# Kernel tuning notes

Measured on AMD Instinct MI355X. Metric: run time of the kernel, lower is better.

The kernel has to match this reference:

```python
import jax, jax.numpy as jnp
import numpy as np
import math

H = 2048      # hidden_size
NH = 32       # num heads
HD = H // NH  # head_dim = 64
THETA = 10000.0
B, S = 2, 2048


def _rope_tables(seq_len):
    inv_freq = 1.0 / (THETA ** (jnp.arange(0, HD, 2, dtype=jnp.float32) / HD))
    t = jnp.arange(seq_len, dtype=jnp.float32)
    freqs = t[:, None] * inv_freq[None, :]          # [S, HD/2]
    emb = jnp.concatenate([freqs, freqs], axis=-1)  # [S, HD]
    return jnp.cos(emb)[None, None], jnp.sin(emb)[None, None]  # [1,1,S,HD]


def _rotate_half(x):
    x1, x2 = jnp.split(x, 2, axis=-1)
    return jnp.concatenate([-x2, x1], axis=-1)


def setup_inputs() -> dict:
    key = jax.random.key(0)
    ks = jax.random.split(key, 5)
    hidden_states = jax.random.normal(ks[0], (B, S, H), dtype=jnp.float32)
    wscale = 1.0 / math.sqrt(H)
    wq = jax.random.normal(ks[1], (H, H), dtype=jnp.float32) * wscale
    wk = jax.random.normal(ks[2], (H, H), dtype=jnp.float32) * wscale
    wv = jax.random.normal(ks[3], (H, H), dtype=jnp.float32) * wscale
    wo = jax.random.normal(ks[4], (H, H), dtype=jnp.float32) * wscale
    # additive causal mask: 0 on/below diagonal, -1e9 above
    causal = jnp.tril(jnp.ones((S, S), dtype=bool))
    attention_mask = jnp.where(causal, 0.0, -1e9).astype(jnp.float32)[None, None]
    return {"hidden_states": hidden_states, "attention_mask": attention_mask,
            "wq": wq, "wk": wk, "wv": wv, "wo": wo}


def reference(hidden_states, attention_mask, wq, wk, wv, wo):
    b, s, _ = hidden_states.shape
    # projections (Linear, no bias); weights stored [in, out]
    q = (hidden_states @ wq).reshape(b, s, NH, HD).transpose(0, 2, 1, 3)  # [B,NH,S,HD]
    k = (hidden_states @ wk).reshape(b, s, NH, HD).transpose(0, 2, 1, 3)
    v = (hidden_states @ wv).reshape(b, s, NH, HD).transpose(0, 2, 1, 3)
    # RoPE
    cos, sin = _rope_tables(s)
    q = q * cos + _rotate_half(q) * sin
    k = k * cos + _rotate_half(k) * sin
    # attention
    attn = jnp.einsum('bhqd,bhkd->bhqk', q, k) / math.sqrt(HD)
    attn = attn + attention_mask
    w = jax.nn.softmax(attn, axis=-1)
    out = jnp.einsum('bhqk,bhkd->bhqd', w, v)           # [B,NH,S,HD]
    out = out.transpose(0, 2, 1, 3).reshape(b, s, H)    # [B,S,H]
    return out @ wo
```

## Files before the change

kernel.cpp:

```cpp
#include <hip/hip_runtime.h>
#include <hip/hip_bf16.h>

#define H 2048
#define NH 32
#define HD 64
#define BB 2
#define SS 2048
#define MM (BB*SS)

typedef __attribute__((ext_vector_type(8))) short bf16x8;
typedef __attribute__((ext_vector_type(4))) float f32x4;
typedef __attribute__((ext_vector_type(16))) float f32x16;
typedef unsigned short u16;
typedef unsigned int u32;
typedef __attribute__((ext_vector_type(4))) u32 u32x4;

static __device__ __forceinline__ u16 f2bf(float f){
  union { float f; u32 i; } v; v.f = f;
  u32 x = v.i;
  return (u16)((x + 0x7FFFu + ((x >> 16) & 1u)) >> 16);
}
static __device__ __forceinline__ float bf2f(u16 u){
  union { u32 i; float f; } v; v.i = ((u32)u) << 16; return v.f;
}
static __device__ __forceinline__ u32 pk2(float a, float b){
  u32 r;
  asm("v_cvt_pk_bf16_f32 %0, %1, %2" : "=v"(r) : "v"(a), "v"(b));
  return r;
}

static __device__ __forceinline__ void gload16(const u16* g, u16* l){
  __builtin_amdgcn_global_load_lds((const __attribute__((address_space(1))) void*)g,
                                   (__attribute__((address_space(3))) void*)l, 16, 0, 0);
}

__global__ void k_cvt(const float* __restrict__ src, u16* __restrict__ dst){
  const int i = (blockIdx.x * 256 + threadIdx.x) * 4;
  float4 v = *(const float4*)(src + i);
  ushort4 o;
  o.x = f2bf(v.x); o.y = f2bf(v.y); o.z = f2bf(v.z); o.w = f2bf(v.w);
  *(ushort4*)(dst + i) = o;
}

__global__ void k_wtrans(const float* __restrict__ w0, const float* __restrict__ w1,
                         const float* __restrict__ w2, const float* __restrict__ w3,
                         u16* __restrict__ d0, u16* __restrict__ d1,
                         u16* __restrict__ d2, u16* __restrict__ d3){
  __shared__ float tile[32][33];
  const int z = blockIdx.z;
  const float* w = z==0 ? w0 : z==1 ? w1 : z==2 ? w2 : w3;
  u16* d        = z==0 ? d0 : z==1 ? d1 : z==2 ? d2 : d3;
  const int n0 = blockIdx.x * 32, k0 = blockIdx.y * 32;
  const int tx = threadIdx.x, ty = threadIdx.y;
  #pragma unroll
  for (int j = 0; j < 4; j++)
    tile[ty + 8*j][tx] = w[(size_t)(k0 + ty + 8*j) * H + n0 + tx];
  __syncthreads();
  #pragma unroll
  for (int j = 0; j < 4; j++)
    d[(size_t)(n0 + ty + 8*j) * H + k0 + tx] = f2bf(tile[tx][ty + 8*j]);
}

__global__ __launch_bounds__(512, 2) void k_gemm8(
    const u16* __restrict__ A, const u16* __restrict__ Bt,
    u16* __restrict__ CQ, u16* __restrict__ CK, u16* __restrict__ CV,
    int M, int K){
  __shared__ __align__(16) u16 As[2][128][64];
  __shared__ __align__(16) u16 Bs[2][384][64];
  const int flat = blockIdx.x;
  const int id = (flat & 7) * 64 + (flat >> 3);
  const int gy = id >> 5, gx = id & 31;
  const int m0 = gx * 128, n0 = gy * 384;
  const int t = threadIdx.x, w = t >> 6, l = t & 63;
  const int wm = w >> 2, wn = w & 3;
  const int lrow = l & 15, lk = (l >> 4) * 8;
  const int sw = (lrow & 7) * 8;
  const int sr = t >> 3, sc = (t & 7) * 8;
  const int ssc = sc ^ ((sr & 7) * 8);
  const int NK = K >> 6;

  auto stageA = [&](int kt, int u){
    const size_t kb = (size_t)kt * 64 + ssc;
    #pragma unroll
    for (int c = 0; c < 2; c++)
      gload16(A + (size_t)(m0 + c*64 + sr) * K + kb, &As[u][c*64 + sr][sc]);
  };
  auto stageB = [&](int kt, int u){
    const size_t kb = (size_t)kt * 64 + ssc;
    #pragma unroll
    for (int c = 0; c < 6; c++)
      gload16(Bt + (size_t)(n0 + c*64 + sr) * K + kb, &Bs[u][c*64 + sr][sc]);
  };

  f32x4 acc[4][6] = {};

  stageA(0, 0); stageB(0, 0);
  stageA(1, 1); stageB(1, 1);
  asm volatile("s_waitcnt vmcnt(8)" ::: "memory");
  __builtin_amdgcn_s_barrier();

  #pragma unroll 1
  for (int kt = 0; kt < NK; ++kt){
    const int u = kt & 1;
    const bool more = (kt + 2 < NK);
    bf16x8 b0[6], b1[6], a0, a1;

    #pragma unroll
    for (int n = 0; n < 6; n++)
      b0[n] = *(const bf16x8*)&Bs[u][wn*96 + n*16 + lrow][lk ^ sw];
    a0 = *(const bf16x8*)&As[u][wm*64 +  0 + lrow][lk ^ sw];
    a1 = *(const bf16x8*)&As[u][wm*64 + 16 + lrow][lk ^ sw];
    __builtin_amdgcn_s_setprio(1);
    #pragma unroll
    for (int n = 0; n < 6; n++){
      acc[0][n] = __builtin_amdgcn_mfma_f32_16x16x32_bf16(a0, b0[n], acc[0][n], 0, 0, 0);
      acc[1][n] = __builtin_amdgcn_mfma_f32_16x16x32_bf16(a1, b0[n], acc[1][n], 0, 0, 0);
    }
    __builtin_amdgcn_s_setprio(0);
    __builtin_amdgcn_s_barrier();

    #pragma unroll
    for (int n = 0; n < 6; n++)
      b1[n] = *(const bf16x8*)&Bs[u][wn*96 + n*16 + lrow][(32 + lk) ^ sw];
    a0 = *(const bf16x8*)&As[u][wm*64 +  0 + lrow][(32 + lk) ^ sw];
    a1 = *(const bf16x8*)&As[u][wm*64 + 16 + lrow][(32 + lk) ^ sw];
    __builtin_amdgcn_s_setprio(1);
    #pragma unroll
    for (int n = 0; n < 6; n++){
      acc[0][n] = __builtin_amdgcn_mfma_f32_16x16x32_bf16(a0, b1[n], acc[0][n], 0, 0, 0);
      acc[1][n] = __builtin_amdgcn_mfma_f32_16x16x32_bf16(a1, b1[n], acc[1][n], 0, 0, 0);
    }
    __builtin_amdgcn_s_setprio(0);
    __builtin_amdgcn_s_barrier();

    if (more) stageB(kt + 2, u);
    a0 = *(const bf16x8*)&As[u][wm*64 + 32 + lrow][lk ^ sw];
    a1 = *(const bf16x8*)&As[u][wm*64 + 48 + lrow][lk ^ sw];
    __builtin_amdgcn_s_setprio(1);
    #pragma unroll
    for (int n = 0; n < 6; n++){
      acc[2][n] = __builtin_amdgcn_mfma_f32_16x16x32_bf16(a0, b0[n], acc[2][n], 0, 0, 0);
      acc[3][n] = __builtin_amdgcn_mfma_f32_16x16x32_bf16(a1, b0[n], acc[3][n], 0, 0, 0);
    }
    __builtin_amdgcn_s_setprio(0);
    __builtin_amdgcn_s_barrier();

    a0 = *(const bf16x8*)&As[u][wm*64 + 32 + lrow][(32 + lk) ^ sw];
    a1 = *(const bf16x8*)&As[u][wm*64 + 48 + lrow][(32 + lk) ^ sw];
    __builtin_amdgcn_s_setprio(1);
    #pragma unroll
    for (int n = 0; n < 6; n++){
      acc[2][n] = __builtin_amdgcn_mfma_f32_16x16x32_bf16(a0, b1[n], acc[2][n], 0, 0, 0);
      acc[3][n] = __builtin_amdgcn_mfma_f32_16x16x32_bf16(a1, b1[n], acc[3][n], 0, 0, 0);
    }
    __builtin_amdgcn_s_setprio(0);
    __builtin_amdgcn_s_barrier();

    if (more){
      stageA(kt + 2, u);
      asm volatile("s_waitcnt vmcnt(8)" ::: "memory");
      __builtin_amdgcn_s_barrier();
    } else if (kt + 1 < NK){
      asm volatile("s_waitcnt vmcnt(0)" ::: "memory");
      __builtin_amdgcn_s_barrier();
    }
  }

  #pragma unroll
  for (int m = 0; m < 4; m++)
    #pragma unroll
    for (int n = 0; n < 6; n++){
      const int ncol = n0 + wn*96 + n*16 + lrow;
      const int z = ncol >> 11;
      u16* C = (z == 0 ? CQ : z == 1 ? CK : CV) + (ncol & 2047);
      #pragma unroll
      for (int r = 0; r < 4; r++){
        const int row = m0 + wm*64 + m*16 + (l >> 4)*4 + r;
        C[(size_t)row * H] = f2bf(acc[m][n][r]);
      }
    }
}

__global__ __launch_bounds__(512, 2) void k_gemmo(
    const u16* __restrict__ A, const u16* __restrict__ Bt,
    float* __restrict__ C, int M, int N, int K){
  __shared__ __align__(16) u16 As[2][128][64];
  __shared__ __align__(16) u16 Bs[2][256][64];
  const int flat = blockIdx.x;
  const int id = (flat & 7) * 32 + (flat >> 3);
  const int gy = id >> 5, gx = id & 31;
  const int m0 = gx * 128, n0 = gy * 256;
  const int t = threadIdx.x, w = t >> 6, l = t & 63;
  const int wm = w >> 2, wn = w & 3;
  const int lrow = l & 15, lk = (l >> 4) * 8;
  const int sw = (lrow & 7) * 8;
  const int sr = t >> 3, sc = (t & 7) * 8;
  const int ssc = sc ^ ((sr & 7) * 8);
  const int NK = K >> 6;

  auto stageA = [&](int kt, int u){
    const size_t kb = (size_t)kt * 64 + ssc;
    #pragma unroll
    for (int c = 0; c < 2; c++)
      gload16(A + (size_t)(m0 + c*64 + sr) * K + kb, &As[u][c*64 + sr][sc]);
  };
  auto stageB = [&](int kt, int u){
    const size_t kb = (size_t)kt * 64 + ssc;
    #pragma unroll
    for (int c = 0; c < 4; c++)
      gload16(Bt + (size_t)(n0 + c*64 + sr) * K + kb, &Bs[u][c*64 + sr][sc]);
  };

  f32x4 acc[4][4] = {};

  stageA(0, 0); stageB(0, 0);
  stageA(1, 1); stageB(1, 1);
  asm volatile("s_waitcnt vmcnt(6)" ::: "memory");
  __builtin_amdgcn_s_barrier();

  #pragma unroll 1
  for (int kt = 0; kt < NK; ++kt){
    const int u = kt & 1;
    const bool more = (kt + 2 < NK);
    bf16x8 b0[4], b1[4], a0, a1;

    #pragma unroll
    for (int n = 0; n < 4; n++)
      b0[n] = *(const bf16x8*)&Bs[u][wn*64 + n*16 + lrow][lk ^ sw];
    a0 = *(const bf16x8*)&As[u][wm*64 +  0 + lrow][lk ^ sw];
    a1 = *(const bf16x8*)&As[u][wm*64 + 16 + lrow][lk ^ sw];
    __builtin_amdgcn_s_setprio(1);
    #pragma unroll
    for (int n = 0; n < 4; n++){
      acc[0][n] = __builtin_amdgcn_mfma_f32_16x16x32_bf16(a0, b0[n], acc[0][n], 0, 0, 0);
      acc[1][n] = __builtin_amdgcn_mfma_f32_16x16x32_bf16(a1, b0[n], acc[1][n], 0, 0, 0);
    }
    __builtin_amdgcn_s_setprio(0);
    __builtin_amdgcn_s_barrier();

    #pragma unroll
    for (int n = 0; n < 4; n++)
      b1[n] = *(const bf16x8*)&Bs[u][wn*64 + n*16 + lrow][(32 + lk) ^ sw];
    a0 = *(const bf16x8*)&As[u][wm*64 +  0 + lrow][(32 + lk) ^ sw];
    a1 = *(const bf16x8*)&As[u][wm*64 + 16 + lrow][(32 + lk) ^ sw];
    __builtin_amdgcn_s_setprio(1);
    #pragma unroll
    for (int n = 0; n < 4; n++){
      acc[0][n] = __builtin_amdgcn_mfma_f32_16x16x32_bf16(a0, b1[n], acc[0][n], 0, 0, 0);
      acc[1][n] = __builtin_amdgcn_mfma_f32_16x16x32_bf16(a1, b1[n], acc[1][n], 0, 0, 0);
    }
    __builtin_amdgcn_s_setprio(0);
    __builtin_amdgcn_s_barrier();

    if (more) stageB(kt + 2, u);
    a0 = *(const bf16x8*)&As[u][wm*64 + 32 + lrow][lk ^ sw];
    a1 = *(const bf16x8*)&As[u][wm*64 + 48 + lrow][lk ^ sw];
    __builtin_amdgcn_s_setprio(1);
    #pragma unroll
    for (int n = 0; n < 4; n++){
      acc[2][n] = __builtin_amdgcn_mfma_f32_16x16x32_bf16(a0, b0[n], acc[2][n], 0, 0, 0);
      acc[3][n] = __builtin_amdgcn_mfma_f32_16x16x32_bf16(a1, b0[n], acc[3][n], 0, 0, 0);
    }
    __builtin_amdgcn_s_setprio(0);
    __builtin_amdgcn_s_barrier();

    a0 = *(const bf16x8*)&As[u][wm*64 + 32 + lrow][(32 + lk) ^ sw];
    a1 = *(const bf16x8*)&As[u][wm*64 + 48 + lrow][(32 + lk) ^ sw];
    __builtin_amdgcn_s_setprio(1);
    #pragma unroll
    for (int n = 0; n < 4; n++){
      acc[2][n] = __builtin_amdgcn_mfma_f32_16x16x32_bf16(a0, b1[n], acc[2][n], 0, 0, 0);
      acc[3][n] = __builtin_amdgcn_mfma_f32_16x16x32_bf16(a1, b1[n], acc[3][n], 0, 0, 0);
    }
    __builtin_amdgcn_s_setprio(0);
    __builtin_amdgcn_s_barrier();

    if (more){
      stageA(kt + 2, u);
      asm volatile("s_waitcnt vmcnt(6)" ::: "memory");
      __builtin_amdgcn_s_barrier();
    } else if (kt + 1 < NK){
      asm volatile("s_waitcnt vmcnt(0)" ::: "memory");
      __builtin_amdgcn_s_barrier();
    }
  }

  #pragma unroll
  for (int m = 0; m < 4; m++)
    #pragma unroll
    for (int n = 0; n < 4; n++){
      const int col = n0 + wn*64 + n*16 + lrow;
      #pragma unroll
      for (int r = 0; r < 4; r++){
        const int row = m0 + wm*64 + m*16 + (l >> 4)*4 + r;
        C[(size_t)row * N + col] = acc[m][n][r];
      }
    }
}

__global__ void k_rope(u16* __restrict__ Kp){
  const int idx = blockIdx.x * 256 + threadIdx.x;
  const int quad = idx & 3;
  const int h = (idx >> 2) & 31;
  const int row = idx >> 7;
  const int s = row & (SS - 1);
  const int i0 = quad * 8;
  u16* k = Kp + (size_t)row * H + h * HD;
  uint4 k1v = *(const uint4*)(k + i0);
  uint4 k2v = *(const uint4*)(k + i0 + 32);
  u16* k1 = (u16*)&k1v; u16* k2 = (u16*)&k2v;
  const float sf = (float)s;
  #pragma unroll
  for (int e = 0; e < 8; e++){
    const int i = i0 + e;
    const float inv = exp2f(-0.4152410118609203f * (float)i);
    float rev = sf * inv * 0.15915494309189535f;
    rev -= floorf(rev);
    const float sn = __builtin_amdgcn_sinf(rev);
    const float cs = __builtin_amdgcn_cosf(rev);
    const float ka = bf2f(k1[e]), kb = bf2f(k2[e]);
    k1[e] = f2bf(ka*cs - kb*sn);
    k2[e] = f2bf(kb*cs + ka*sn);
  }
  *(uint4*)(k + i0)      = k1v;
  *(uint4*)(k + i0 + 32) = k2v;
}

__global__ __launch_bounds__(256, 2) void k_attn(
    const u16* __restrict__ Q, const u16* __restrict__ K,
    const u16* __restrict__ V, u16* __restrict__ O){
  __shared__ __align__(16) u16 Ks[3][64][64];
  __shared__ __align__(16) u16 Vs[2][64][72];
  const int t = threadIdx.x, w = t >> 6, l = t & 63;
  const int x = blockIdx.x, bh = blockIdx.y;
  const int b = bh >> 5, h = bh & 31;
  const u16* kp = K + (size_t)(b*SS) * H + h * HD;
  const u16* vp = V + (size_t)(b*SS) * H + h * HD;
  const int sr = t >> 3, sc = (t & 7) * 8;
  const int ssc = sc ^ ((sr & 7) * 8);
  const int hi = l >> 5, lq = l & 31;
  const float QSC = 0.18033688011112042f;

  auto stageK = [&](int tile, int buf){
    const int jb = tile * 64;
    gload16(kp + (size_t)(jb + sr) * H + ssc,      &Ks[buf][sr][sc]);
    gload16(kp + (size_t)(jb + 32 + sr) * H + ssc, &Ks[buf][32 + sr][sc]);
  };
  auto loadV = [&](int tile, uint4* vv){
    const int jb = tile * 64;
    vv[0] = *(const uint4*)(vp + (size_t)(jb + sr) * H + sc);
    vv[1] = *(const uint4*)(vp + (size_t)(jb + 32 + sr) * H + sc);
  };
  auto publishV = [&](const uint4* vv, int buf){
    #pragma unroll
    for (int c = 0; c < 2; c++){
      const int j = c*32 + sr;
      const u16* pv = (const u16*)&vv[c];
      #pragma unroll
      for (int e = 0; e < 8; e++){
        const int d = sc + e;
        Vs[buf][d][j ^ ((d >> 3) * 8)] = pv[e];
      }
    }
  };

  #pragma unroll 1
  for (int pp = 0; pp < 2; pp++){
    const int qt = pp ? x : (15 - x);
    const int NT = 2*qt + 2;
    const int qw0 = qt*128 + w*32;
    const int qrow = qw0 + lq;

    const u16* qptr = Q + (size_t)(b*SS + qrow) * H + h * HD + hi*8;
    bf16x8 qr0 = *(const bf16x8*)(qptr + 0);
    bf16x8 qr1 = *(const bf16x8*)(qptr + 16);
    bf16x8 qr2 = *(const bf16x8*)(qptr + 32);
    bf16x8 qr3 = *(const bf16x8*)(qptr + 48);
    bf16x8 qf[4];
    {
      const float sf = (float)qrow;
      #pragma unroll
      for (int e = 0; e < 8; e++){
        #pragma unroll
        for (int pr = 0; pr < 2; pr++){
          const int d = pr*16 + hi*8 + e;
          const float inv = exp2f(-0.4152410118609203f * (float)d);
          float rev = sf * inv * 0.15915494309189535f;
          rev -= floorf(rev);
          const float sn = __builtin_amdgcn_sinf(rev);
          const float cs = __builtin_amdgcn_cosf(rev);
          const float qa = bf2f((u16)(pr ? qr1[e] : qr0[e]));
          const float qb = bf2f((u16)(pr ? qr3[e] : qr2[e]));
          const u16 oa = f2bf((qa*cs - qb*sn) * QSC);
          const u16 ob = f2bf((qb*cs + qa*sn) * QSC);
          if (pr){ qf[1][e] = (short)oa; qf[3][e] = (short)ob; }
          else   { qf[0][e] = (short)oa; qf[2][e] = (short)ob; }
        }
      }
    }

    float mrun = -1e30f, lrun = 0.f;
    f32x16 oacc[2] = {};
    uint4 vvE[2], vvO[2];

    stageK(0, 0); loadV(0, vvE);
    stageK(1, 1); loadV(1, vvO);
    asm volatile("s_waitcnt vmcnt(4)" ::: "memory");
    publishV(vvE, 0);
    asm volatile("s_waitcnt lgkmcnt(0)" ::: "memory");
    __builtin_amdgcn_s_barrier();

    auto body = [&](int jt, int p, uint4* vvSelf, const uint4* vvOther){
      const int j0 = jt * 64;
      if (jt + 2 < NT){ stageK(jt + 2, (jt + 2) % 3); loadV(jt + 2, vvSelf); }

      if (j0 <= qw0){
        const int kbuf = jt % 3;
        f32x16 sv[2] = {};
        __builtin_amdgcn_s_setprio(1);
        #pragma unroll
        for (int kb = 0; kb < 2; kb++){
          const int row = kb*32 + lq;
          #pragma unroll
          for (int c = 0; c < 4; c++){
            bf16x8 kf = *(const bf16x8*)&Ks[kbuf][row][(c*16 + hi*8) ^ ((row & 7) * 8)];
            sv[kb] = __builtin_amdgcn_mfma_f32_32x32x16_bf16(kf, qf[c], sv[kb], 0, 0, 0);
          }
        }
        __builtin_amdgcn_s_setprio(0);
        if (j0 + 63 > qw0){
          #pragma unroll
          for (int kb = 0; kb < 2; kb++)
            #pragma unroll
            for (int r = 0; r < 16; r++){
              const int kg = j0 + kb*32 + (r & 3) + 8*(r >> 2) + 4*hi;
              if (kg > qrow) sv[kb][r] = -1e30f;
            }
        }
        float t16[16], t8[8], t4[4];
        #pragma unroll
        for (int r = 0; r < 16; r++) t16[r] = fmaxf(sv[0][r], sv[1][r]);
        #pragma unroll
        for (int r = 0; r < 8; r++) t8[r] = fmaxf(t16[r], t16[r+8]);
        #pragma unroll
        for (int r = 0; r < 4; r++) t4[r] = fmaxf(t8[r], t8[r+4]);
        float tm = fmaxf(fmaxf(t4[0], t4[2]), fmaxf(t4[1], t4[3]));
        tm = fmaxf(tm, __shfl_xor(tm, 32, 64));
        if (__any(tm > mrun)){
          const float mn = fmaxf(mrun, tm);
          const float fac = exp2f(mrun - mn);
          mrun = mn;
          lrun *= fac;
          #pragma unroll
          for (int db = 0; db < 2; db++)
            #pragma unroll
            for (int r = 0; r < 16; r++) oacc[db][r] *= fac;
        }
        #pragma unroll
        for (int kb = 0; kb < 2; kb++)
          #pragma unroll
          for (int r = 0; r < 16; r++) sv[kb][r] = exp2f(sv[kb][r] - mrun);
        float s16[16], s8[8], s4[4];
        #pragma unroll
        for (int r = 0; r < 16; r++) s16[r] = sv[0][r] + sv[1][r];
        #pragma unroll
        for (int r = 0; r < 8; r++) s8[r] = s16[r] + s16[r+8];
        #pragma unroll
        for (int r = 0; r < 4; r++) s4[r] = s8[r] + s8[r+4];
        float rs = (s4[0] + s4[1]) + (s4[2] + s4[3]);
        rs += __shfl_xor(rs, 32, 64);
        lrun += rs;
        u32x4 pw[4];
        #pragma unroll
        for (int kb = 0; kb < 2; kb++){
          #pragma unroll
          for (int half = 0; half < 2; half++){
            const int rb = half * 8;
            const u32 own0 = pk2(sv[kb][rb+0], sv[kb][rb+1]);
            const u32 own1 = pk2(sv[kb][rb+2], sv[kb][rb+3]);
            const u32 own2 = pk2(sv[kb][rb+4], sv[kb][rb+5]);
            const u32 own3 = pk2(sv[kb][rb+6], sv[kb][rb+7]);
            const u32 s0 = hi ? own0 : own2;
            const u32 s1 = hi ? own1 : own3;
            const u32 r0 = __shfl_xor(s0, 32, 64);
            const u32 r1 = __shfl_xor(s1, 32, 64);
            u32x4 pv;
            pv[0] = hi ? r0 : own0;
            pv[1] = hi ? r1 : own1;
            pv[2] = hi ? own2 : r0;
            pv[3] = hi ? own3 : r1;
            pw[kb*2 + half] = pv;
          }
        }
        __builtin_amdgcn_s_setprio(1);
        #pragma unroll
        for (int db = 0; db < 2; db++){
          const int d = db*32 + lq;
          #pragma unroll
          for (int tt = 0; tt < 4; tt++){
            bf16x8 vf = *(const bf16x8*)&Vs[p][d][(tt*16 + hi*8) ^ ((d >> 3) * 8)];
            bf16x8 pfr = __builtin_bit_cast(bf16x8, pw[tt]);
            oacc[db] = __builtin_amdgcn_mfma_f32_32x32x16_bf16(vf, pfr, oacc[db], 0, 0, 0);
          }
        }
        __builtin_amdgcn_s_setprio(0);
      }

      if (jt + 2 < NT) asm volatile("s_waitcnt vmcnt(4)" ::: "memory");
      else             asm volatile("s_waitcnt vmcnt(0)" ::: "memory");
      if (jt + 1 < NT) publishV(vvOther, p ^ 1);
      asm volatile("s_waitcnt lgkmcnt(0)" ::: "memory");
      __builtin_amdgcn_s_barrier();
    };

    #pragma unroll 1
    for (int jt2 = 0; jt2 < NT; jt2 += 2){
      body(jt2,     0, vvE, vvO);
      body(jt2 + 1, 1, vvO, vvE);
    }

    const float rl = 1.0f / lrun;
    u16* op = O + (size_t)(b*SS + qrow) * H + h * HD;
    #pragma unroll
    for (int db = 0; db < 2; db++)
      #pragma unroll
      for (int rq = 0; rq < 4; rq++){
        ushort4 o4;
        o4.x = f2bf(oacc[db][rq*4 + 0] * rl);
        o4.y = f2bf(oacc[db][rq*4 + 1] * rl);
        o4.z = f2bf(oacc[db][rq*4 + 2] * rl);
        o4.w = f2bf(oacc[db][rq*4 + 3] * rl);
        *(ushort4*)(op + db*32 + rq*8 + 4*hi) = o4;
      }
  }
}

extern "C" void kernel_launch(void* const* d_in, const int* in_sizes, int n_in,
                              void* d_out, int out_size, void* d_ws, size_t ws_size,
                              hipStream_t stream){
  (void)in_sizes; (void)n_in; (void)out_size; (void)ws_size;
  const float* hs = (const float*)d_in[0];
  const float* wq = (const float*)d_in[2];
  const float* wk = (const float*)d_in[3];
  const float* wv = (const float*)d_in[4];
  const float* wo = (const float*)d_in[5];
  float* out = (float*)d_out;
  char* ws = (char*)d_ws;

  u16* Xb  = (u16*)ws;
  u16* Wqt = (u16*)(ws + (size_t)MM * H * 2);
  u16* Wkt = Wqt + (size_t)H * H;
  u16* Wvt = Wkt + (size_t)H * H;
  u16* Wot = Wvt + (size_t)H * H;
  u16* Vb  = Wot + (size_t)H * H;
  u16* Ob  = Vb  + (size_t)MM * H;
  u16* Qb  = (u16*)d_out;
  u16* Kb  = Qb + (size_t)MM * H;

  k_cvt<<<8192, 256, 0, stream>>>(hs, Xb);
  k_wtrans<<<dim3(64, 64, 4), dim3(32, 8), 0, stream>>>(wq, wk, wv, wo, Wqt, Wkt, Wvt, Wot);
  k_gemm8<<<512, 512, 0, stream>>>(Xb, Wqt, Qb, Kb, Vb, MM, H);
  k_rope<<<2048, 256, 0, stream>>>(Kb);
  k_attn<<<dim3(8, 64), 256, 0, stream>>>(Qb, Kb, Vb, Ob);
  k_gemmo<<<256, 512, 0, stream>>>(Ob, Wot, out, MM, H, H);
}
```

Before: 287.8 us.

## Retile QKV GEMM to 256x256 blocks with register-prefetched B fragments

The fused QKV projection GEMM moves from 128x384 tiles over 512 blocks to 256x256 tiles over 384 blocks, with each wave computing a 128x64 sub-tile. That raises arithmetic intensity per LDS byte and cuts global reloads of A and B. The K loop becomes a two-stage ping-pong body: A is staged one step ahead and B two steps ahead in halves, and the first B fragments for the next step are prefetched into registers. The aim is to overlap loads with MFMA work while using fewer, larger blocks. The trade-off is more accumulator registers, 384 blocks that may not fill the CUs evenly, and more barriers per iteration.

```diff
diff --git a/kernel.cpp b/kernel.cpp
--- a/kernel.cpp
+++ b/kernel.cpp
@@ -14,6 +14,8 @@
 typedef unsigned short u16;
 typedef unsigned int u32;
 typedef __attribute__((ext_vector_type(4))) u32 u32x4;
+
+#define MFMA16(acc, av, bv) acc = __builtin_amdgcn_mfma_f32_16x16x32_bf16(av, bv, acc, 0, 0, 0)
 
 static __device__ __forceinline__ u16 f2bf(float f){
   union { float f; u32 i; } v; v.f = f;
@@ -65,12 +67,12 @@
     const u16* __restrict__ A, const u16* __restrict__ Bt,
     u16* __restrict__ CQ, u16* __restrict__ CK, u16* __restrict__ CV,
     int M, int K){
-  __shared__ __align__(16) u16 As[2][128][64];
-  __shared__ __align__(16) u16 Bs[2][384][64];
+  __shared__ __align__(16) u16 As[2][256][64];
+  __shared__ __align__(16) u16 Bs[2][256][64];
   const int flat = blockIdx.x;
-  const int id = (flat & 7) * 64 + (flat >> 3);
-  const int gy = id >> 5, gx = id & 31;
-  const int m0 = gx * 128, n0 = gy * 384;
+  const int id = (flat & 7) * 48 + (flat >> 3);
+  const int gx = id & 15, gy = id >> 4;
+  const int m0 = gx * 256, n0 = gy * 256;
   const int t = threadIdx.x, w = t >> 6, l = t & 63;
   const int wm = w >> 2, wn = w & 3;
   const int lrow = l & 15, lk = (l >> 4) * 8;
@@ -79,103 +81,150 @@
   const int ssc = sc ^ ((sr & 7) * 8);
   const int NK = K >> 6;
 
-  auto stageA = [&](int kt, int u){
+  auto stA = [&](int kt, int half){
+    const int u = kt & 1;
     const size_t kb = (size_t)kt * 64 + ssc;
     #pragma unroll
     for (int c = 0; c < 2; c++)
-      gload16(A + (size_t)(m0 + c*64 + sr) * K + kb, &As[u][c*64 + sr][sc]);
-  };
-  auto stageB = [&](int kt, int u){
+      gload16(A + (size_t)(m0 + half*128 + c*64 + sr) * K + kb,
+              &As[u][half*128 + c*64 + sr][sc]);
+  };
+  auto stB = [&](int kt, int half){
+    const int u = kt & 1;
     const size_t kb = (size_t)kt * 64 + ssc;
     #pragma unroll
-    for (int c = 0; c < 6; c++)
-      gload16(Bt + (size_t)(n0 + c*64 + sr) * K + kb, &Bs[u][c*64 + sr][sc]);
-  };
-
-  f32x4 acc[4][6] = {};
-
-  stageA(0, 0); stageB(0, 0);
-  stageA(1, 1); stageB(1, 1);
-  asm volatile("s_waitcnt vmcnt(8)" ::: "memory");
+    for (int c = 0; c < 2; c++)
+      gload16(Bt + (size_t)(n0 + half*128 + c*64 + sr) * K + kb,
+              &Bs[u][half*128 + c*64 + sr][sc]);
+  };
+
+  f32x4 acc[8][4] = {};
+  bf16x8 bcE[2][2], bcO[2][2];
+
+  stA(0, 0); stA(0, 1); stB(0, 0); stB(0, 1);
+  stB(1, 0); stB(1, 1);
+  asm volatile("s_waitcnt vmcnt(4)" ::: "memory");
   __builtin_amdgcn_s_barrier();
+  #pragma unroll
+  for (int n = 0; n < 2; n++)
+    #pragma unroll
+    for (int kk = 0; kk < 2; kk++)
+      bcE[n][kk] = *(const bf16x8*)&Bs[0][wn*64 + n*16 + lrow][(kk*32 + lk) ^ sw];
+
+  auto body = [&](int kt, bf16x8 (&bcur)[2][2], bf16x8 (&bnxt)[2][2]){
+    const int u = kt & 1;
+    const bool h1 = (kt + 1 < NK), h2 = (kt + 2 < NK);
+    bf16x8 a[4][2], b23[2][2];
+
+    #pragma unroll
+    for (int m = 0; m < 4; m++)
+      #pragma unroll
+      for (int kk = 0; kk < 2; kk++)
+        a[m][kk] = *(const bf16x8*)&As[u][wm*128 + m*16 + lrow][(kk*32 + lk) ^ sw];
+    if (h1) stA(kt + 1, 0);
+    __builtin_amdgcn_sched_barrier(0);
+    __builtin_amdgcn_s_barrier();
+    asm volatile("s_waitcnt lgkmcnt(0)" ::: "memory");
+    __builtin_amdgcn_sched_barrier(0);
+    __builtin_amdgcn_s_setprio(1);
+    #pragma unroll
+    for (int m = 0; m < 4; m++)
+      #pragma unroll
+      for (int n = 0; n < 2; n++){
+        MFMA16(acc[m][n], a[m][0], bcur[n][0]);
+        MFMA16(acc[m][n], a[m][1], bcur[n][1]);
+      }
+    __builtin_amdgcn_s_setprio(0);
+    __builtin_amdgcn_s_barrier();
+
+    #pragma unroll
+    for (int n = 0; n < 2; n++)
+      #pragma unroll
+      for (int kk = 0; kk < 2; kk++)
+        b23[n][kk] = *(const bf16x8*)&Bs[u][wn*64 + (2+n)*16 + lrow][(kk*32 + lk) ^ sw];
+    if (h1) stA(kt + 1, 1);
+    __builtin_amdgcn_sched_barrier(0);
+    __builtin_amdgcn_s_barrier();
+    asm volatile("s_waitcnt lgkmcnt(0)" ::: "memory");
+    __builtin_amdgcn_sched_barrier(0);
+    __builtin_amdgcn_s_setprio(1);
+    #pragma unroll
+    for (int m = 0; m < 4; m++)
+      #pragma unroll
+      for (int n = 0; n < 2; n++){
+        MFMA16(acc[m][2+n], a[m][0], b23[n][0]);
+        MFMA16(acc[m][2+n], a[m][1], b23[n][1]);
+      }
+    __builtin_amdgcn_s_setprio(0);
+    __builtin_amdgcn_s_barrier();
+
+    #pragma unroll
+    for (int m = 0; m < 4; m++)
+      #pragma unroll
+      for (int kk = 0; kk < 2; kk++)
+        a[m][kk] = *(const bf16x8*)&As[u][wm*128 + 64 + m*16 + lrow][(kk*32 + lk) ^ sw];
+    if (h2) stB(kt + 2, 0);
+    __builtin_amdgcn_sched_barrier(0);
+    __builtin_amdgcn_s_barrier();
+    asm volatile("s_waitcnt lgkmcnt(0)" ::: "memory");
+    __builtin_amdgcn_sched_barrier(0);
+    __builtin_amdgcn_s_setprio(1);
+    #pragma unroll
+    for (int m = 0; m < 4; m++)
+      #pragma unroll
+      for (int n = 0; n < 2; n++){
+        MFMA16(acc[4+m][2+n], a[m][0], b23[n][0]);
+        MFMA16(acc[4+m][2+n], a[m][1], b23[n][1]);
+      }
+    __builtin_amdgcn_s_setprio(0);
+    if (h2)      asm volatile("s_waitcnt vmcnt(6)" ::: "memory");
+    else if (h1) asm volatile("s_waitcnt vmcnt(4)" ::: "memory");
+    __builtin_amdgcn_s_barrier();
+
+    if (h1){
+      #pragma unroll
+      for (int n = 0; n < 2; n++)
+        #pragma unroll
+        for (int kk = 0; kk < 2; kk++)
+          bnxt[n][kk] = *(const bf16x8*)&Bs[u ^ 1][wn*64 + n*16 + lrow][(kk*32 + lk) ^ sw];
+    }
+    if (h2) stB(kt + 2, 1);
+    __builtin_amdgcn_sched_barrier(0);
+    __builtin_amdgcn_s_barrier();
+    asm volatile("s_waitcnt lgkmcnt(0)" ::: "memory");
+    __builtin_amdgcn_sched_barrier(0);
+    __builtin_amdgcn_s_setprio(1);
+    #pragma unroll
+    for (int m = 0; m < 4; m++)
+      #pragma unroll
+      for (int n = 0; n < 2; n++){
+        MFMA16(acc[4+m][n], a[m][0], bcur[n][0]);
+        MFMA16(acc[4+m][n], a[m][1], bcur[n][1]);
+      }
+    __builtin_amdgcn_s_setprio(0);
+    __builtin_amdgcn_s_barrier();
+
+    if (h2) asm volatile("s_waitcnt vmcnt(4)" ::: "memory");
+    else    asm volatile("s_waitcnt vmcnt(0)" ::: "memory");
+    __builtin_amdgcn_s_barrier();
+  };
 
   #pragma unroll 1
-  for (int kt = 0; kt < NK; ++kt){
-    const int u = kt & 1;
-    const bool more = (kt + 2 < NK);
-    bf16x8 b0[6], b1[6], a0, a1;
-
-    #pragma unroll
-    for (int n = 0; n < 6; n++)
-      b0[n] = *(const bf16x8*)&Bs[u][wn*96 + n*16 + lrow][lk ^ sw];
-    a0 = *(const bf16x8*)&As[u][wm*64 +  0 + lrow][lk ^ sw];
-    a1 = *(const bf16x8*)&As[u][wm*64 + 16 + lrow][lk ^ sw];
-    __builtin_amdgcn_s_setprio(1);
-    #pragma unroll
-    for (int n = 0; n < 6; n++){
-      acc[0][n] = __builtin_amdgcn_mfma_f32_16x16x32_bf16(a0, b0[n], acc[0][n], 0, 0, 0);
-      acc[1][n] = __builtin_amdgcn_mfma_f32_16x16x32_bf16(a1, b0[n], acc[1][n], 0, 0, 0);
-    }
-    __builtin_amdgcn_s_setprio(0);
-    __builtin_amdgcn_s_barrier();
-
-    #pragma unroll
-    for (int n = 0; n < 6; n++)
-      b1[n] = *(const bf16x8*)&Bs[u][wn*96 + n*16 + lrow][(32 + lk) ^ sw];
-    a0 = *(const bf16x8*)&As[u][wm*64 +  0 + lrow][(32 + lk) ^ sw];
-    a1 = *(const bf16x8*)&As[u][wm*64 + 16 + lrow][(32 + lk) ^ sw];
-    __builtin_amdgcn_s_setprio(1);
-    #pragma unroll
-    for (int n = 0; n < 6; n++){
-      acc[0][n] = __builtin_amdgcn_mfma_f32_16x16x32_bf16(a0, b1[n], acc[0][n], 0, 0, 0);
-      acc[1][n] = __builtin_amdgcn_mfma_f32_16x16x32_bf16(a1, b1[n], acc[1][n], 0, 0, 0);
-    }
-    __builtin_amdgcn_s_setprio(0);
-    __builtin_amdgcn_s_barrier();
-
-    if (more) stageB(kt + 2, u);
-    a0 = *(const bf16x8*)&As[u][wm*64 + 32 + lrow][lk ^ sw];
-    a1 = *(const bf16x8*)&As[u][wm*64 + 48 + lrow][lk ^ sw];
-    __builtin_amdgcn_s_setprio(1);
-    #pragma unroll
-    for (int n = 0; n < 6; n++){
-      acc[2][n] = __builtin_amdgcn_mfma_f32_16x16x32_bf16(a0, b0[n], acc[2][n], 0, 0, 0);
-      acc[3][n] = __builtin_amdgcn_mfma_f32_16x16x32_bf16(a1, b0[n], acc[3][n], 0, 0, 0);
-    }
-    __builtin_amdgcn_s_setprio(0);
-    __builtin_amdgcn_s_barrier();
-
-    a0 = *(const bf16x8*)&As[u][wm*64 + 32 + lrow][(32 + lk) ^ sw];
-    a1 = *(const bf16x8*)&As[u][wm*64 + 48 + lrow][(32 + lk) ^ sw];
-    __builtin_amdgcn_s_setprio(1);
-    #pragma unroll
-    for (int n = 0; n < 6; n++){
-      acc[2][n] = __builtin_amdgcn_mfma_f32_16x16x32_bf16(a0, b1[n], acc[2][n], 0, 0, 0);
-      acc[3][n] = __builtin_amdgcn_mfma_f32_16x16x32_bf16(a1, b1[n], acc[3][n], 0, 0, 0);
-    }
-    __builtin_amdgcn_s_setprio(0);
-    __builtin_amdgcn_s_barrier();
-
-    if (more){
-      stageA(kt + 2, u);
-      asm volatile("s_waitcnt vmcnt(8)" ::: "memory");
-      __builtin_amdgcn_s_barrier();
-    } else if (kt + 1 < NK){
-      asm volatile("s_waitcnt vmcnt(0)" ::: "memory");
-      __builtin_amdgcn_s_barrier();
-    }
+  for (int kt = 0; kt < NK; kt += 2){
+    body(kt,     bcE, bcO);
+    body(kt + 1, bcO, bcE);
   }
 
   #pragma unroll
-  for (int m = 0; m < 4; m++)
-    #pragma unroll
-    for (int n = 0; n < 6; n++){
-      const int ncol = n0 + wn*96 + n*16 + lrow;
+  for (int m = 0; m < 8; m++)
+    #pragma unroll
+    for (int n = 0; n < 4; n++){
+      const int ncol = n0 + wn*64 + n*16 + lrow;
       const int z = ncol >> 11;
       u16* C = (z == 0 ? CQ : z == 1 ? CK : CV) + (ncol & 2047);
       #pragma unroll
       for (int r = 0; r < 4; r++){
-        const int row = m0 + wm*64 + m*16 + (l >> 4)*4 + r;
+        const int row = m0 + wm*128 + m*16 + (l >> 4)*4 + r;
         C[(size_t)row * H] = f2bf(acc[m][n][r]);
       }
     }
@@ -232,8 +281,8 @@
     __builtin_amdgcn_s_setprio(1);
     #pragma unroll
     for (int n = 0; n < 4; n++){
-      acc[0][n] = __builtin_amdgcn_mfma_f32_16x16x32_bf16(a0, b0[n], acc[0][n], 0, 0, 0);
-      acc[1][n] = __builtin_amdgcn_mfma_f32_16x16x32_bf16(a1, b0[n], acc[1][n], 0, 0, 0);
+      MFMA16(acc[0][n], a0, b0[n]);
+      MFMA16(acc[1][n], a1, b0[n]);
     }
     __builtin_amdgcn_s_setprio(0);
     __builtin_amdgcn_s_barrier();
@@ -246,8 +295,8 @@
     __builtin_amdgcn_s_setprio(1);
     #pragma unroll
     for (int n = 0; n < 4; n++){
-      acc[0][n] = __builtin_amdgcn_mfma_f32_16x16x32_bf16(a0, b1[n], acc[0][n], 0, 0, 0);
-      acc[1][n] = __builtin_amdgcn_mfma_f32_16x16x32_bf16(a1, b1[n], acc[1][n], 0, 0, 0);
+      MFMA16(acc[0][n], a0, b1[n]);
+      MFMA16(acc[1][n], a1, b1[n]);
     }
     __builtin_amdgcn_s_setprio(0);
     __builtin_amdgcn_s_barrier();
@@ -258,8 +307,8 @@
     __builtin_amdgcn_s_setprio(1);
     #pragma unroll
     for (int n = 0; n < 4; n++){
-      acc[2][n] = __builtin_amdgcn_mfma_f32_16x16x32_bf16(a0, b0[n], acc[2][n], 0, 0, 0);
-      acc[3][n] = __builtin_amdgcn_mfma_f32_16x16x32_bf16(a1, b0[n], acc[3][n], 0, 0, 0);
+      MFMA16(acc[2][n], a0, b0[n]);
+      MFMA16(acc[3][n], a1, b0[n]);
     }
     __builtin_amdgcn_s_setprio(0);
     __builtin_amdgcn_s_barrier();
@@ -269,8 +318,8 @@
     __builtin_amdgcn_s_setprio(1);
     #pragma unroll
     for (int n = 0; n < 4; n++){
-      acc[2][n] = __builtin_amdgcn_mfma_f32_16x16x32_bf16(a0, b1[n], acc[2][n], 0, 0, 0);
-      acc[3][n] = __builtin_amdgcn_mfma_f32_16x16x32_bf16(a1, b1[n], acc[3][n], 0, 0, 0);
+      MFMA16(acc[2][n], a0, b1[n]);
+      MFMA16(acc[3][n], a1, b1[n]);
     }
     __builtin_amdgcn_s_setprio(0);
     __builtin_amdgcn_s_barrier();
@@ -559,7 +608,7 @@
 
   k_cvt<<<8192, 256, 0, stream>>>(hs, Xb);
   k_wtrans<<<dim3(64, 64, 4), dim3(32, 8), 0, stream>>>(wq, wk, wv, wo, Wqt, Wkt, Wvt, Wot);
-  k_gemm8<<<512, 512, 0, stream>>>(Xb, Wqt, Qb, Kb, Vb, MM, H);
+  k_gemm8<<<384, 512, 0, stream>>>(Xb, Wqt, Qb, Kb, Vb, MM, H);
   k_rope<<<2048, 256, 0, stream>>>(Kb);
   k_attn<<<dim3(8, 64), 256, 0, stream>>>(Qb, Kb, Vb, Ob);
   k_gemmo<<<256, 512, 0, stream>>>(Ob, Wot, out, MM, H, H);
```

After: 295.2 us. +2.6%, slower.

## Enlarge attention query tile to 256 rows with 512-thread blocks

Applied to the files above, without the earlier changes.

The attention kernel now uses 8 waves per block (512 threads), each covering 32 query rows, so every block handles a 256-row query tile instead of 128. Each K/V tile loaded into shared memory is reused by twice as many waves, and each thread stages one row of K and V instead of two. The grid shrinks to 4 query-tile pairs per batch-head, and the causal pairing becomes (7-x, x). In exchange, the block count drops and more warps wait at each barrier, which may hurt occupancy and load balance. The GEMM change only introduces an MFMA macro and is cosmetic.

```diff
diff --git a/kernel.cpp b/kernel.cpp
--- a/kernel.cpp
+++ b/kernel.cpp
@@ -14,6 +14,8 @@
 typedef unsigned short u16;
 typedef unsigned int u32;
 typedef __attribute__((ext_vector_type(4))) u32 u32x4;
+
+#define MFMA16(acc, av, bv) acc = __builtin_amdgcn_mfma_f32_16x16x32_bf16(av, bv, acc, 0, 0, 0)
 
 static __device__ __forceinline__ u16 f2bf(float f){
   union { float f; u32 i; } v; v.f = f;
@@ -113,8 +115,8 @@
     __builtin_amdgcn_s_setprio(1);
     #pragma unroll
     for (int n = 0; n < 6; n++){
-      acc[0][n] = __builtin_amdgcn_mfma_f32_16x16x32_bf16(a0, b0[n], acc[0][n], 0, 0, 0);
-      acc[1][n] = __builtin_amdgcn_mfma_f32_16x16x32_bf16(a1, b0[n], acc[1][n], 0, 0, 0);
+      MFMA16(acc[0][n], a0, b0[n]);
+      MFMA16(acc[1][n], a1, b0[n]);
     }
     __builtin_amdgcn_s_setprio(0);
     __builtin_amdgcn_s_barrier();
@@ -127,8 +129,8 @@
     __builtin_amdgcn_s_setprio(1);
     #pragma unroll
     for (int n = 0; n < 6; n++){
-      acc[0][n] = __builtin_amdgcn_mfma_f32_16x16x32_bf16(a0, b1[n], acc[0][n], 0, 0, 0);
-      acc[1][n] = __builtin_amdgcn_mfma_f32_16x16x32_bf16(a1, b1[n], acc[1][n], 0, 0, 0);
+      MFMA16(acc[0][n], a0, b1[n]);
+      MFMA16(acc[1][n], a1, b1[n]);
     }
     __builtin_amdgcn_s_setprio(0);
     __builtin_amdgcn_s_barrier();
@@ -139,8 +141,8 @@
     __builtin_amdgcn_s_setprio(1);
     #pragma unroll
     for (int n = 0; n < 6; n++){
-      acc[2][n] = __builtin_amdgcn_mfma_f32_16x16x32_bf16(a0, b0[n], acc[2][n], 0, 0, 0);
-      acc[3][n] = __builtin_amdgcn_mfma_f32_16x16x32_bf16(a1, b0[n], acc[3][n], 0, 0, 0);
+      MFMA16(acc[2][n], a0, b0[n]);
+      MFMA16(acc[3][n], a1, b0[n]);
     }
     __builtin_amdgcn_s_setprio(0);
     __builtin_amdgcn_s_barrier();
@@ -150,8 +152,8 @@
     __builtin_amdgcn_s_setprio(1);
     #pragma unroll
     for (int n = 0; n < 6; n++){
-      acc[2][n] = __builtin_amdgcn_mfma_f32_16x16x32_bf16(a0, b1[n], acc[2][n], 0, 0, 0);
-      acc[3][n] = __builtin_amdgcn_mfma_f32_16x16x32_bf16(a1, b1[n], acc[3][n], 0, 0, 0);
+      MFMA16(acc[2][n], a0, b1[n]);
+      MFMA16(acc[3][n], a1, b1[n]);
     }
     __builtin_amdgcn_s_setprio(0);
     __builtin_amdgcn_s_barrier();
@@ -232,8 +234,8 @@
     __builtin_amdgcn_s_setprio(1);
     #pragma unroll
     for (int n = 0; n < 4; n++){
-      acc[0][n] = __builtin_amdgcn_mfma_f32_16x16x32_bf16(a0, b0[n], acc[0][n], 0, 0, 0);
-      acc[1][n] = __builtin_amdgcn_mfma_f32_16x16x32_bf16(a1, b0[n], acc[1][n], 0, 0, 0);
+      MFMA16(acc[0][n], a0, b0[n]);
+      MFMA16(acc[1][n], a1, b0[n]);
     }
     __builtin_amdgcn_s_setprio(0);
     __builtin_amdgcn_s_barrier();
@@ -246,8 +248,8 @@
     __builtin_amdgcn_s_setprio(1);
     #pragma unroll
     for (int n = 0; n < 4; n++){
-      acc[0][n] = __builtin_amdgcn_mfma_f32_16x16x32_bf16(a0, b1[n], acc[0][n], 0, 0, 0);
-      acc[1][n] = __builtin_amdgcn_mfma_f32_16x16x32_bf16(a1, b1[n], acc[1][n], 0, 0, 0);
+      MFMA16(acc[0][n], a0, b1[n]);
+      MFMA16(acc[1][n], a1, b1[n]);
     }
     __builtin_amdgcn_s_setprio(0);
     __builtin_amdgcn_s_barrier();
@@ -258,8 +260,8 @@
     __builtin_amdgcn_s_setprio(1);
     #pragma unroll
     for (int n = 0; n < 4; n++){
-      acc[2][n] = __builtin_amdgcn_mfma_f32_16x16x32_bf16(a0, b0[n], acc[2][n], 0, 0, 0);
-      acc[3][n] = __builtin_amdgcn_mfma_f32_16x16x32_bf16(a1, b0[n], acc[3][n], 0, 0, 0);
+      MFMA16(acc[2][n], a0, b0[n]);
+      MFMA16(acc[3][n], a1, b0[n]);
     }
     __builtin_amdgcn_s_setprio(0);
     __builtin_amdgcn_s_barrier();
@@ -269,8 +271,8 @@
     __builtin_amdgcn_s_setprio(1);
     #pragma unroll
     for (int n = 0; n < 4; n++){
-      acc[2][n] = __builtin_amdgcn_mfma_f32_16x16x32_bf16(a0, b1[n], acc[2][n], 0, 0, 0);
-      acc[3][n] = __builtin_amdgcn_mfma_f32_16x16x32_bf16(a1, b1[n], acc[3][n], 0, 0, 0);
+      MFMA16(acc[2][n], a0, b1[n]);
+      MFMA16(acc[3][n], a1, b1[n]);
     }
     __builtin_amdgcn_s_setprio(0);
     __builtin_amdgcn_s_barrier();
@@ -326,7 +328,7 @@
   *(uint4*)(k + i0 + 32) = k2v;
 }
 
-__global__ __launch_bounds__(256, 2) void k_attn(
+__global__ __launch_bounds__(512, 2) void k_attn(
     const u16* __restrict__ Q, const u16* __restrict__ K,
     const u16* __restrict__ V, u16* __restrict__ O){
   __shared__ __align__(16) u16 Ks[3][64][64];
@@ -342,33 +344,25 @@
   const float QSC = 0.18033688011112042f;
 
   auto stageK = [&](int tile, int buf){
-    const int jb = tile * 64;
-    gload16(kp + (size_t)(jb + sr) * H + ssc,      &Ks[buf][sr][sc]);
-    gload16(kp + (size_t)(jb + 32 + sr) * H + ssc, &Ks[buf][32 + sr][sc]);
-  };
-  auto loadV = [&](int tile, uint4* vv){
-    const int jb = tile * 64;
-    vv[0] = *(const uint4*)(vp + (size_t)(jb + sr) * H + sc);
-    vv[1] = *(const uint4*)(vp + (size_t)(jb + 32 + sr) * H + sc);
-  };
-  auto publishV = [&](const uint4* vv, int buf){
-    #pragma unroll
-    for (int c = 0; c < 2; c++){
-      const int j = c*32 + sr;
-      const u16* pv = (const u16*)&vv[c];
-      #pragma unroll
-      for (int e = 0; e < 8; e++){
-        const int d = sc + e;
-        Vs[buf][d][j ^ ((d >> 3) * 8)] = pv[e];
-      }
+    gload16(kp + (size_t)(tile*64 + sr) * H + ssc, &Ks[buf][sr][sc]);
+  };
+  auto loadV = [&](int tile, uint4& vv){
+    vv = *(const uint4*)(vp + (size_t)(tile*64 + sr) * H + sc);
+  };
+  auto publishV = [&](const uint4& vv, int buf){
+    const u16* pv = (const u16*)&vv;
+    #pragma unroll
+    for (int e = 0; e < 8; e++){
+      const int d = sc + e;
+      Vs[buf][d][sr ^ ((d >> 3) * 8)] = pv[e];
     }
   };
 
   #pragma unroll 1
   for (int pp = 0; pp < 2; pp++){
-    const int qt = pp ? x : (15 - x);
-    const int NT = 2*qt + 2;
-    const int qw0 = qt*128 + w*32;
+    const int qt = pp ? x : (7 - x);
+    const int NT = 4*qt + 4;
+    const int qw0 = qt*256 + w*32;
     const int qrow = qw0 + lq;
 
     const u16* qptr = Q + (size_t)(b*SS + qrow) * H + h * HD + hi*8;
@@ -401,16 +395,16 @@
 
     float mrun = -1e30f, lrun = 0.f;
     f32x16 oacc[2] = {};
-    uint4 vvE[2], vvO[2];
+    uint4 vvE, vvO;
 
     stageK(0, 0); loadV(0, vvE);
     stageK(1, 1); loadV(1, vvO);
-    asm volatile("s_waitcnt vmcnt(4)" ::: "memory");
+    asm volatile("s_waitcnt vmcnt(2)" ::: "memory");
     publishV(vvE, 0);
     asm volatile("s_waitcnt lgkmcnt(0)" ::: "memory");
     __builtin_amdgcn_s_barrier();
 
-    auto body = [&](int jt, int p, uint4* vvSelf, const uint4* vvOther){
+    auto body = [&](int jt, int p, uint4& vvSelf, const uint4& vvOther){
       const int j0 = jt * 64;
       if (jt + 2 < NT){ stageK(jt + 2, (jt + 2) % 3); loadV(jt + 2, vvSelf); }
 
@@ -506,7 +500,7 @@
         __builtin_amdgcn_s_setprio(0);
       }
 
-      if (jt + 2 < NT) asm volatile("s_waitcnt vmcnt(4)" ::: "memory");
+      if (jt + 2 < NT) asm volatile("s_waitcnt vmcnt(2)" ::: "memory");
       else             asm volatile("s_waitcnt vmcnt(0)" ::: "memory");
       if (jt + 1 < NT) publishV(vvOther, p ^ 1);
       asm volatile("s_waitcnt lgkmcnt(0)" ::: "memory");
@@ -561,6 +555,6 @@
   k_wtrans<<<dim3(64, 64, 4), dim3(32, 8), 0, stream>>>(wq, wk, wv, wo, Wqt, Wkt, Wvt, Wot);
   k_gemm8<<<512, 512, 0, stream>>>(Xb, Wqt, Qb, Kb, Vb, MM, H);
   k_rope<<<2048, 256, 0, stream>>>(Kb);
-  k_attn<<<dim3(8, 64), 256, 0, stream>>>(Qb, Kb, Vb, Ob);
+  k_attn<<<dim3(4, 64), 512, 0, stream>>>(Qb, Kb, Vb, Ob);
   k_gemmo<<<256, 512, 0, stream>>>(Ob, Wot, out, MM, H, H);
 }
```

Measured after the change: 292.8 us. No clear change (+1.7%).
